# Kernel optimization log

Hardware: AMD Instinct MI355X
Metric: run time of the kernel (lower is better)

The kernel has to match this reference:

```python
import jax, jax.numpy as jnp
import numpy as np

B, T, EPROJS, DUNITS, ATT_DIM = 32, 2048, 512, 512, 512
ACONV_CHANS, ACONV_FILT = 32, 100
SCALING = 2.0


def _lin(k, fan_in, fan_out):
    k1, k2 = jax.random.split(k)
    lim = 1.0 / np.sqrt(fan_in)
    w = jax.random.uniform(k1, (fan_in, fan_out), minval=-lim, maxval=lim, dtype=jnp.float32)
    b = jax.random.uniform(k2, (fan_out,), minval=-lim, maxval=lim, dtype=jnp.float32)
    return w, b


def setup_inputs() -> dict:
    key = jax.random.key(0)
    ks = jax.random.split(key, 16)
    W_w, W_b = _lin(ks[0], DUNITS, ATT_DIM)
    V_w, V_b = _lin(ks[1], EPROJS, ATT_DIM)
    U_w, U_b = _lin(ks[2], DUNITS, ATT_DIM)
    g_w, g_b = _lin(ks[3], ATT_DIM, 1)
    K = 2 * ACONV_FILT + 1
    lim = 1.0 / np.sqrt(K)
    conv_w = jax.random.uniform(ks[4], (ACONV_CHANS, 1, K), minval=-lim, maxval=lim, dtype=jnp.float32)
    lim = 1.0 / np.sqrt(ATT_DIM)
    W_ih = jax.random.uniform(ks[5], (4 * ATT_DIM, ACONV_CHANS), minval=-lim, maxval=lim, dtype=jnp.float32)
    W_hh = jax.random.uniform(ks[6], (4 * ATT_DIM, ATT_DIM), minval=-lim, maxval=lim, dtype=jnp.float32)
    b_ih = jax.random.uniform(ks[7], (4 * ATT_DIM,), minval=-lim, maxval=lim, dtype=jnp.float32)
    b_hh = jax.random.uniform(ks[8], (4 * ATT_DIM,), minval=-lim, maxval=lim, dtype=jnp.float32)
    enc_hs_pad = jax.random.normal(ks[9], (B, T, EPROJS), dtype=jnp.float32)
    enc_hs_len = jax.random.randint(ks[10], (B,), T // 2, T + 1, dtype=jnp.int32)
    dec_z = jax.random.normal(ks[11], (B, DUNITS), dtype=jnp.float32)
    att_prev = jax.random.uniform(ks[12], (B, T), dtype=jnp.float32)
    att_h = jax.random.normal(ks[13], (B, ATT_DIM), dtype=jnp.float32)
    att_c = jax.random.normal(ks[14], (B, ATT_DIM), dtype=jnp.float32)
    return dict(enc_hs_pad=enc_hs_pad, enc_hs_len=enc_hs_len, dec_z=dec_z,
                att_prev=att_prev, att_h=att_h, att_c=att_c,
                W_w=W_w, W_b=W_b, V_w=V_w, V_b=V_b, U_w=U_w, U_b=U_b,
                g_w=g_w, g_b=g_b, conv_w=conv_w,
                W_ih=W_ih, W_hh=W_hh, b_ih=b_ih, b_hh=b_hh)


def reference(enc_hs_pad, enc_hs_len, dec_z, att_prev, att_h, att_c,
              W_w, W_b, V_w, V_b, U_w, U_b, g_w, g_b, conv_w,
              W_ih, W_hh, b_ih, b_hh):
    # pre-computed encoder projection: (B, T, att_dim)
    pre = jnp.einsum('bte,ea->bta', enc_hs_pad, V_w) + V_b
    # location conv over previous attention weights: (B, C, T)
    conv = jax.lax.conv_general_dilated(att_prev[:, None, :], conv_w,
                                        window_strides=(1,),
                                        padding=[(ACONV_FILT, ACONV_FILT)],
                                        dimension_numbers=('NCH', 'OIH', 'NCH'))
    feat = jnp.max(jax.nn.relu(conv), axis=-1)  # (B, C): max-pool over time
    # LSTMCell (torch gate order: i, f, g, o)
    gates = feat @ W_ih.T + b_ih + att_h @ W_hh.T + b_hh
    i, f, g, o = jnp.split(gates, 4, axis=-1)
    c_new = jax.nn.sigmoid(f) * att_c + jax.nn.sigmoid(i) * jnp.tanh(g)
    h_new = jax.nn.sigmoid(o) * jnp.tanh(c_new)
    # additive score
    dec_proj = dec_z @ U_w + U_b            # (B, att_dim)
    wh = h_new @ W_w + W_b                  # (B, att_dim)
    e = jnp.tanh(wh[:, None, :] + pre + dec_proj[:, None, :])  # (B, T, att_dim)
    score = jnp.einsum('bta,a->bt', e, g_w[:, 0]) + g_b[0]     # (B, T)
    mask = jnp.arange(T)[None, :] >= enc_hs_len[:, None]
    score = jnp.where(mask, jnp.asarray(-1e30, score.dtype), score)
    w = jax.nn.softmax(SCALING * score, axis=1)
    c_v = jnp.einsum('bte,bt->be', enc_hs_pad, w)  # (B, eprojs)
    return c_v, w, h_new, c_new
```

## Files before the change

kernel.cpp:

```cpp
#include <hip/hip_runtime.h>
#include <math.h>

#define BB 32
#define TT_SEQ 2048
#define EPROJS 512
#define ATT 512
#define NCH 32
#define FILT 100
#define KCONV 201
#define G4 2048

typedef unsigned short ushort_t;
typedef unsigned int uint_t;
typedef __attribute__((ext_vector_type(8))) short bf16x8_t;
typedef __attribute__((ext_vector_type(4))) float f32x4_t;

__device__ inline ushort_t f2bf(float f) {
    uint_t u = __float_as_uint(f);
    uint_t r = (u + 0x7fffu + ((u >> 16) & 1u)) >> 16;
    return (ushort_t)r;
}

__device__ inline float tanh_fast(float x) {
    float e = __expf(2.0f * x);
    return 1.0f - 2.0f / (e + 1.0f);
}

__global__ __launch_bounds__(256) void k_conv(const float* __restrict__ att_prev,
                                              const float* __restrict__ conv_w,
                                              float* __restrict__ feat) {
    int b = blockIdx.x >> 5;
    int c = blockIdx.x & 31;
    __shared__ float row[TT_SEQ + 2 * FILT];
    __shared__ float wsh[KCONV];
    __shared__ float red[4];
    for (int i = threadIdx.x; i < TT_SEQ + 2 * FILT; i += 256) {
        int t = i - FILT;
        row[i] = (t >= 0 && t < TT_SEQ) ? att_prev[b * TT_SEQ + t] : 0.0f;
    }
    for (int i = threadIdx.x; i < KCONV; i += 256) wsh[i] = conv_w[c * KCONV + i];
    __syncthreads();
    float m = 0.0f;
    for (int t = threadIdx.x; t < TT_SEQ; t += 256) {
        float s = 0.0f;
        #pragma unroll 4
        for (int k = 0; k < KCONV; ++k) s = fmaf(wsh[k], row[t + k], s);
        m = fmaxf(m, s);
    }
    #pragma unroll
    for (int off = 32; off; off >>= 1) m = fmaxf(m, __shfl_xor(m, off, 64));
    if ((threadIdx.x & 63) == 0) red[threadIdx.x >> 6] = m;
    __syncthreads();
    if (threadIdx.x == 0) {
        m = fmaxf(fmaxf(red[0], red[1]), fmaxf(red[2], red[3]));
        feat[b * NCH + c] = m;
    }
}

#define HP 518
__global__ __launch_bounds__(256) void k_gates(const float* __restrict__ feat,
                                               const float* __restrict__ att_h,
                                               const float* __restrict__ W_ih,
                                               const float* __restrict__ W_hh,
                                               const float* __restrict__ b_ih,
                                               const float* __restrict__ b_hh,
                                               float* __restrict__ gates) {
    __shared__ float hsh[32 * HP];
    __shared__ float fsh[32 * 33];
    int tid = threadIdx.x;
    for (int i = tid; i < 32 * 512; i += 256) {
        int r = i >> 9, c = i & 511;
        hsh[r * HP + c] = att_h[i];
    }
    for (int i = tid; i < 1024; i += 256) fsh[(i >> 5) * 33 + (i & 31)] = feat[i];
    __syncthreads();
    int jl = tid >> 5, b = tid & 31;
    int j = blockIdx.x * 8 + jl;
    float acc = b_ih[j] + b_hh[j];
    const float4* wi = (const float4*)(W_ih + (size_t)j * NCH);
    #pragma unroll
    for (int k4 = 0; k4 < 8; ++k4) {
        float4 w = wi[k4];
        const float* f = fsh + b * 33 + k4 * 4;
        acc = fmaf(w.x, f[0], acc);
        acc = fmaf(w.y, f[1], acc);
        acc = fmaf(w.z, f[2], acc);
        acc = fmaf(w.w, f[3], acc);
    }
    const float4* wh = (const float4*)(W_hh + (size_t)j * ATT);
    float a0 = 0.f, a1 = 0.f, a2 = 0.f, a3 = 0.f;
    #pragma unroll 8
    for (int k4 = 0; k4 < 128; ++k4) {
        float4 w = wh[k4];
        float2 h0 = *(const float2*)(hsh + b * HP + k4 * 4);
        float2 h1 = *(const float2*)(hsh + b * HP + k4 * 4 + 2);
        a0 = fmaf(w.x, h0.x, a0);
        a1 = fmaf(w.y, h0.y, a1);
        a2 = fmaf(w.z, h1.x, a2);
        a3 = fmaf(w.w, h1.y, a3);
    }
    gates[(size_t)b * G4 + j] = acc + ((a0 + a1) + (a2 + a3));
}

__global__ __launch_bounds__(256) void k_lstm_elem(const float* __restrict__ gates,
                                                   const float* __restrict__ att_c,
                                                   float* __restrict__ h_out,
                                                   float* __restrict__ c_out) {
    int i = blockIdx.x * 256 + threadIdx.x;
    int b = i >> 9, a = i & 511;
    const float* g = gates + (size_t)b * G4;
    float ig = g[a], fg = g[ATT + a], gg = g[2 * ATT + a], og = g[3 * ATT + a];
    float si = 1.0f / (1.0f + expf(-ig));
    float sf = 1.0f / (1.0f + expf(-fg));
    float so = 1.0f / (1.0f + expf(-og));
    float cn = sf * att_c[i] + si * tanhf(gg);
    float hn = so * tanhf(cn);
    c_out[i] = cn;
    h_out[i] = hn;
}

__global__ __launch_bounds__(256) void k_addvec_par(const float* __restrict__ dec_z,
                                                    const float* __restrict__ h_new,
                                                    const float* __restrict__ U_w,
                                                    const float* __restrict__ W_w,
                                                    float* __restrict__ add_vec) {
    int a0 = blockIdx.x * 32;
    int k0 = blockIdx.y * 64;
    __shared__ float zsh[32 * 65];
    __shared__ float hsh[32 * 65];
    __shared__ float us[64 * 33];
    __shared__ float ws2[64 * 33];
    int tid = threadIdx.x;
    for (int i = tid; i < 2048; i += 256) {
        int b = i >> 6, d = i & 63;
        zsh[b * 65 + d] = dec_z[(size_t)b * ATT + k0 + d];
        hsh[b * 65 + d] = h_new[(size_t)b * ATT + k0 + d];
        int dr = i >> 5, c = i & 31;
        us[dr * 33 + c] = U_w[(size_t)(k0 + dr) * ATT + a0 + c];
        ws2[dr * 33 + c] = W_w[(size_t)(k0 + dr) * ATT + a0 + c];
    }
    __syncthreads();
    int al = tid >> 5, b = tid & 31;
    float acc[4] = {0.f, 0.f, 0.f, 0.f};
    for (int d = 0; d < 64; ++d) {
        float zv = zsh[b * 65 + d];
        float hv = hsh[b * 65 + d];
        #pragma unroll
        for (int m = 0; m < 4; ++m) {
            int a = al + 8 * m;
            acc[m] = fmaf(zv, us[d * 33 + a], acc[m]);
            acc[m] = fmaf(hv, ws2[d * 33 + a], acc[m]);
        }
    }
    #pragma unroll
    for (int m = 0; m < 4; ++m)
        atomicAdd(&add_vec[(size_t)b * ATT + a0 + al + 8 * m], acc[m]);
}

__global__ __launch_bounds__(256) void k_cvt(const float* __restrict__ src,
                                             ushort_t* __restrict__ dst,
                                             float* __restrict__ score) {
    size_t i = (size_t)blockIdx.x * 256 + threadIdx.x;
    float4 v = ((const float4*)src)[i];
    ushort4 o;
    o.x = f2bf(v.x); o.y = f2bf(v.y); o.z = f2bf(v.z); o.w = f2bf(v.w);
    ((ushort4*)dst)[i] = o;
    if (i < BB * TT_SEQ) score[i] = 0.0f;
}

__global__ __launch_bounds__(256) void k_cvtw(const float* __restrict__ vw,
                                              ushort_t* __restrict__ vwt,
                                              const float* __restrict__ U_b,
                                              const float* __restrict__ W_b,
                                              const float* __restrict__ V_b,
                                              float* __restrict__ add_vec) {
    __shared__ float tile[64][65];
    int eb = blockIdx.x * 64, ab = blockIdx.y * 64;
    for (int it = 0; it < 16; ++it) {
        int idx = threadIdx.x + it * 256;
        int r = idx >> 6, c = idx & 63;
        tile[r][c] = vw[(size_t)(eb + r) * ATT + ab + c];
    }
    __syncthreads();
    for (int it = 0; it < 16; ++it) {
        int idx = threadIdx.x + it * 256;
        int r = idx >> 6, c = idx & 63;
        vwt[(size_t)(ab + r) * EPROJS + eb + c] = f2bf(tile[c][r]);
    }
    int blk = blockIdx.y * 8 + blockIdx.x;
    int i = blk * 256 + threadIdx.x;
    int a = i & 511;
    add_vec[i] = U_b[a] + W_b[a] + V_b[a];
}

__global__ __launch_bounds__(256) void k_gemm_score(
        const ushort_t* __restrict__ Abf,
        const ushort_t* __restrict__ Btbf,
        const float* __restrict__ add_vec,
        const float* __restrict__ g_w,
        const int* __restrict__ lens,
        float* __restrict__ score) {
    int mtile = blockIdx.x;
    int b = mtile >> 4;
    int t0 = (mtile & 15) * 128;
    if (t0 >= lens[b]) return;
    int n0 = blockIdx.y * 128;

    __shared__ __align__(16) ushort_t sA[128 * 64];
    __shared__ __align__(16) ushort_t sB[128 * 64];
    __shared__ float sred[128];

    int tid = threadIdx.x;
    int lane = tid & 63;
    int wave = tid >> 6;
    int wm = wave >> 1, wn = wave & 1;
    int q = lane >> 4, l15 = lane & 15;

    if (tid < 128) sred[tid] = 0.0f;

    const ushort_t* Agbase = Abf + (size_t)mtile * 128 * EPROJS;
    const ushort_t* Bgbase = Btbf + (size_t)n0 * EPROJS;

    f32x4_t acc[4][4];
    #pragma unroll
    for (int i = 0; i < 4; ++i)
        #pragma unroll
        for (int j = 0; j < 4; ++j) acc[i][j] = (f32x4_t){0.f, 0.f, 0.f, 0.f};

    for (int kc = 0; kc < 8; ++kc) {
        __syncthreads();
        #pragma unroll
        for (int it = 0; it < 4; ++it) {
            int g = tid + it * 256;
            int m = g >> 3;
            int kq = g & 7;
            int kqs = kq ^ (m & 7);
            __builtin_amdgcn_global_load_lds(
                (const __attribute__((address_space(1))) void*)(Agbase + (size_t)m * EPROJS + kc * 64 + kqs * 8),
                (__attribute__((address_space(3))) void*)(sA + g * 8), 16, 0, 0);
            __builtin_amdgcn_global_load_lds(
                (const __attribute__((address_space(1))) void*)(Bgbase + (size_t)m * EPROJS + kc * 64 + kqs * 8),
                (__attribute__((address_space(3))) void*)(sB + g * 8), 16, 0, 0);
        }
        __syncthreads();
        #pragma unroll
        for (int s = 0; s < 2; ++s) {
            bf16x8_t af[4], bfr[4];
            int kq = s * 4 + q;
            #pragma unroll
            for (int i = 0; i < 4; ++i) {
                int m = wm * 64 + i * 16 + l15;
                af[i] = *(const bf16x8_t*)(sA + (m * 8 + (kq ^ (m & 7))) * 8);
            }
            #pragma unroll
            for (int j = 0; j < 4; ++j) {
                int n = wn * 64 + j * 16 + l15;
                bfr[j] = *(const bf16x8_t*)(sB + (n * 8 + (kq ^ (n & 7))) * 8);
            }
            #pragma unroll
            for (int i = 0; i < 4; ++i)
                #pragma unroll
                for (int j = 0; j < 4; ++j)
                    acc[i][j] = __builtin_amdgcn_mfma_f32_16x16x32_bf16(af[i], bfr[j], acc[i][j], 0, 0, 0);
        }
    }

    float g4[4], av4[4];
    #pragma unroll
    for (int j = 0; j < 4; ++j) {
        int a = n0 + wn * 64 + j * 16 + l15;
        g4[j] = g_w[a];
        av4[j] = add_vec[b * ATT + a];
    }
    float s_ir[4][4];
    #pragma unroll
    for (int i = 0; i < 4; ++i) {
        #pragma unroll
        for (int r = 0; r < 4; ++r) {
            float s = 0.0f;
            #pragma unroll
            for (int j = 0; j < 4; ++j) {
                float x = acc[i][j][r] + av4[j];
                s = fmaf(g4[j], tanh_fast(x), s);
            }
            s_ir[i][r] = s;
        }
    }
    #pragma unroll
    for (int off = 8; off; off >>= 1) {
        #pragma unroll
        for (int i = 0; i < 4; ++i)
            #pragma unroll
            for (int r = 0; r < 4; ++r)
                s_ir[i][r] += __shfl_xor(s_ir[i][r], off, 16);
    }
    if (l15 == 0) {
        #pragma unroll
        for (int i = 0; i < 4; ++i)
            #pragma unroll
            for (int r = 0; r < 4; ++r)
                atomicAdd(&sred[wm * 64 + i * 16 + q * 4 + r], s_ir[i][r]);
    }
    __syncthreads();
    if (tid < 128) atomicAdd(&score[b * TT_SEQ + t0 + tid], sred[tid]);
}

__global__ __launch_bounds__(256) void k_softmax(const float* __restrict__ score,
                                                 const int* __restrict__ lens,
                                                 float* __restrict__ w_out,
                                                 float* __restrict__ c_v) {
    int b = blockIdx.x;
    int len = lens[b];
    __shared__ float red[4];
    float vals[8];
    float m = -INFINITY;
    #pragma unroll
    for (int i = 0; i < 8; ++i) {
        int t = threadIdx.x + i * 256;
        float s = (t < len) ? 2.0f * score[b * TT_SEQ + t] : -INFINITY;
        vals[i] = s;
        m = fmaxf(m, s);
    }
    #pragma unroll
    for (int off = 32; off; off >>= 1) m = fmaxf(m, __shfl_xor(m, off, 64));
    if ((threadIdx.x & 63) == 0) red[threadIdx.x >> 6] = m;
    __syncthreads();
    m = fmaxf(fmaxf(red[0], red[1]), fmaxf(red[2], red[3]));
    __syncthreads();
    float sum = 0.0f;
    #pragma unroll
    for (int i = 0; i < 8; ++i) {
        float e = expf(vals[i] - m);
        vals[i] = e;
        sum += e;
    }
    #pragma unroll
    for (int off = 32; off; off >>= 1) sum += __shfl_xor(sum, off, 64);
    if ((threadIdx.x & 63) == 0) red[threadIdx.x >> 6] = sum;
    __syncthreads();
    sum = red[0] + red[1] + red[2] + red[3];
    float inv = 1.0f / sum;
    #pragma unroll
    for (int i = 0; i < 8; ++i) w_out[b * TT_SEQ + threadIdx.x + i * 256] = vals[i] * inv;
    for (int i = threadIdx.x; i < EPROJS; i += 256) c_v[b * EPROJS + i] = 0.0f;
}

__global__ __launch_bounds__(256) void k_ctx_bf(const ushort_t* __restrict__ encb,
                                                const float* __restrict__ w,
                                                const int* __restrict__ lens,
                                                float* __restrict__ c_v) {
    int b = blockIdx.y;
    int t0 = blockIdx.x * 128;
    if (t0 >= lens[b]) return;
    __shared__ float wsh[128];
    if (threadIdx.x < 128) wsh[threadIdx.x] = w[b * TT_SEQ + t0 + threadIdx.x];
    __syncthreads();
    const uint_t* base = (const uint_t*)(encb + ((size_t)b * TT_SEQ + t0) * EPROJS);
    float a0 = 0.f, a1 = 0.f;
    for (int t = 0; t < 128; ++t) {
        uint_t u = base[t * 256 + threadIdx.x];
        float lo = __uint_as_float(u << 16);
        float hi = __uint_as_float(u & 0xffff0000u);
        a0 = fmaf(wsh[t], lo, a0);
        a1 = fmaf(wsh[t], hi, a1);
    }
    atomicAdd(&c_v[b * EPROJS + 2 * threadIdx.x], a0);
    atomicAdd(&c_v[b * EPROJS + 2 * threadIdx.x + 1], a1);
}

__global__ __launch_bounds__(256) void k_lstm(const float* __restrict__ feat,
                                              const float* __restrict__ att_h,
                                              const float* __restrict__ att_c,
                                              const float* __restrict__ W_ih,
                                              const float* __restrict__ W_hh,
                                              const float* __restrict__ b_ih,
                                              const float* __restrict__ b_hh,
                                              float* __restrict__ h_out,
                                              float* __restrict__ c_out) {
    int b = blockIdx.x;
    __shared__ float fsh[NCH];
    __shared__ float hsh[ATT];
    __shared__ float gsh[G4];
    if (threadIdx.x < NCH) fsh[threadIdx.x] = feat[b * NCH + threadIdx.x];
    for (int i = threadIdx.x; i < ATT; i += 256) hsh[i] = att_h[b * ATT + i];
    __syncthreads();
    for (int j = threadIdx.x; j < G4; j += 256) {
        float acc = b_ih[j] + b_hh[j];
        const float* wi = W_ih + (size_t)j * NCH;
        #pragma unroll
        for (int c = 0; c < NCH; ++c) acc = fmaf(fsh[c], wi[c], acc);
        const float* wh = W_hh + (size_t)j * ATT;
        for (int a = 0; a < ATT; a += 4) {
            float4 w4 = *(const float4*)(wh + a);
            acc = fmaf(hsh[a + 0], w4.x, acc);
            acc = fmaf(hsh[a + 1], w4.y, acc);
            acc = fmaf(hsh[a + 2], w4.z, acc);
            acc = fmaf(hsh[a + 3], w4.w, acc);
        }
        gsh[j] = acc;
    }
    __syncthreads();
    for (int a = threadIdx.x; a < ATT; a += 256) {
        float ig = gsh[a], fg = gsh[ATT + a], gg = gsh[2 * ATT + a], og = gsh[3 * ATT + a];
        float si = 1.0f / (1.0f + expf(-ig));
        float sf = 1.0f / (1.0f + expf(-fg));
        float so = 1.0f / (1.0f + expf(-og));
        float cn = sf * att_c[b * ATT + a] + si * tanhf(gg);
        float hn = so * tanhf(cn);
        c_out[b * ATT + a] = cn;
        h_out[b * ATT + a] = hn;
    }
}

__global__ __launch_bounds__(256) void k_addvec(const float* __restrict__ dec_z,
                                                const float* __restrict__ h_new,
                                                const float* __restrict__ U_w,
                                                const float* __restrict__ U_b,
                                                const float* __restrict__ W_w,
                                                const float* __restrict__ W_b,
                                                const float* __restrict__ V_b,
                                                float* __restrict__ add_vec) {
    int b = blockIdx.x;
    __shared__ float zsh[ATT];
    __shared__ float hsh[ATT];
    for (int i = threadIdx.x; i < ATT; i += 256) {
        zsh[i] = dec_z[b * ATT + i];
        hsh[i] = h_new[b * ATT + i];
    }
    __syncthreads();
    for (int a = threadIdx.x; a < ATT; a += 256) {
        float acc = U_b[a] + W_b[a] + V_b[a];
        for (int d = 0; d < ATT; ++d) {
            acc = fmaf(zsh[d], U_w[(size_t)d * ATT + a], acc);
            acc = fmaf(hsh[d], W_w[(size_t)d * ATT + a], acc);
        }
        add_vec[b * ATT + a] = acc;
    }
}

#define TTILE 16
#define SR 516
__global__ __launch_bounds__(256) void k_score(const float* __restrict__ enc,
                                               const float* __restrict__ V_w,
                                               const float* __restrict__ add_vec,
                                               const float* __restrict__ g_w,
                                               const float* __restrict__ g_b,
                                               const int* __restrict__ lens,
                                               float* __restrict__ score) {
    int b = blockIdx.y;
    int t0 = blockIdx.x * TTILE;
    int len = lens[b];
    if (t0 >= len) return;
    __shared__ float enc_t[TTILE * SR];
    __shared__ float ash[ATT];
    __shared__ float gwsh[ATT];
    const float* src = enc + ((size_t)b * TT_SEQ + t0) * EPROJS;
    for (int i = threadIdx.x; i < TTILE * 128; i += 256) {
        int r = i >> 7, c4 = (i & 127) << 2;
        *(float4*)(enc_t + r * SR + c4) = *(const float4*)(src + (size_t)r * EPROJS + c4);
    }
    for (int i = threadIdx.x; i < ATT; i += 256) {
        ash[i] = add_vec[b * ATT + i];
        gwsh[i] = g_w[i];
    }
    __syncthreads();
    int t = threadIdx.x >> 4;
    int al = threadIdx.x & 15;
    const float* er = enc_t + t * SR;
    float sc = 0.0f;
    #pragma unroll
    for (int c = 0; c < 2; ++c) {
        float4 acc0 = {0, 0, 0, 0}, acc1 = {0, 0, 0, 0}, acc2 = {0, 0, 0, 0}, acc3 = {0, 0, 0, 0};
        int abase = c * 256 + al * 4;
        const float* vp = V_w + abase;
        for (int e = 0; e < EPROJS; ++e) {
            float s = er[e];
            const float* rowp = vp + (size_t)e * ATT;
            float4 w0 = *(const float4*)(rowp);
            float4 w1 = *(const float4*)(rowp + 64);
            float4 w2 = *(const float4*)(rowp + 128);
            float4 w3 = *(const float4*)(rowp + 192);
            acc0.x = fmaf(s, w0.x, acc0.x); acc0.y = fmaf(s, w0.y, acc0.y);
            acc0.z = fmaf(s, w0.z, acc0.z); acc0.w = fmaf(s, w0.w, acc0.w);
            acc1.x = fmaf(s, w1.x, acc1.x); acc1.y = fmaf(s, w1.y, acc1.y);
            acc1.z = fmaf(s, w1.z, acc1.z); acc1.w = fmaf(s, w1.w, acc1.w);
            acc2.x = fmaf(s, w2.x, acc2.x); acc2.y = fmaf(s, w2.y, acc2.y);
            acc2.z = fmaf(s, w2.z, acc2.z); acc2.w = fmaf(s, w2.w, acc2.w);
            acc3.x = fmaf(s, w3.x, acc3.x); acc3.y = fmaf(s, w3.y, acc3.y);
            acc3.z = fmaf(s, w3.z, acc3.z); acc3.w = fmaf(s, w3.w, acc3.w);
        }
        float av[16] = {acc0.x, acc0.y, acc0.z, acc0.w,
                        acc1.x, acc1.y, acc1.z, acc1.w,
                        acc2.x, acc2.y, acc2.z, acc2.w,
                        acc3.x, acc3.y, acc3.z, acc3.w};
        #pragma unroll
        for (int k = 0; k < 16; ++k) {
            int a = abase + (k >> 2) * 64 + (k & 3);
            sc = fmaf(gwsh[a], tanhf(av[k] + ash[a]), sc);
        }
    }
    #pragma unroll
    for (int off = 8; off; off >>= 1) sc += __shfl_xor(sc, off, 16);
    if (al == 0) score[b * TT_SEQ + t0 + t] = sc + g_b[0];
}

__global__ __launch_bounds__(256) void k_ctx(const float* __restrict__ enc,
                                             const float* __restrict__ w,
                                             const int* __restrict__ lens,
                                             float* __restrict__ c_v) {
    int b = blockIdx.y;
    int t0 = blockIdx.x * 128;
    if (t0 >= lens[b]) return;
    __shared__ float wsh[128];
    if (threadIdx.x < 128) wsh[threadIdx.x] = w[b * TT_SEQ + t0 + threadIdx.x];
    __syncthreads();
    float a0 = 0.0f, a1 = 0.0f;
    const float* base = enc + ((size_t)b * TT_SEQ + t0) * EPROJS;
    for (int t = 0; t < 128; ++t) {
        float wt = wsh[t];
        a0 = fmaf(wt, base[(size_t)t * EPROJS + threadIdx.x], a0);
        a1 = fmaf(wt, base[(size_t)t * EPROJS + threadIdx.x + 256], a1);
    }
    atomicAdd(&c_v[b * EPROJS + threadIdx.x], a0);
    atomicAdd(&c_v[b * EPROJS + threadIdx.x + 256], a1);
}

extern "C" void kernel_launch(void* const* d_in, const int* in_sizes, int n_in,
                              void* d_out, int out_size, void* d_ws, size_t ws_size,
                              hipStream_t stream) {
    const float* enc      = (const float*)d_in[0];
    const int*   lens     = (const int*)d_in[1];
    const float* dec_z    = (const float*)d_in[2];
    const float* att_prev = (const float*)d_in[3];
    const float* att_h    = (const float*)d_in[4];
    const float* att_c    = (const float*)d_in[5];
    const float* W_w      = (const float*)d_in[6];
    const float* W_b      = (const float*)d_in[7];
    const float* V_w      = (const float*)d_in[8];
    const float* V_b      = (const float*)d_in[9];
    const float* U_w      = (const float*)d_in[10];
    const float* U_b      = (const float*)d_in[11];
    const float* g_w      = (const float*)d_in[12];
    const float* g_b      = (const float*)d_in[13];
    const float* conv_w   = (const float*)d_in[14];
    const float* W_ih     = (const float*)d_in[15];
    const float* W_hh     = (const float*)d_in[16];
    const float* b_ih     = (const float*)d_in[17];
    const float* b_hh     = (const float*)d_in[18];

    float* out   = (float*)d_out;
    float* c_v   = out;
    float* w_out = out + BB * EPROJS;
    float* h_out = w_out + BB * TT_SEQ;
    float* c_out = h_out + BB * ATT;

    const size_t ENC_N = (size_t)BB * TT_SEQ * EPROJS;
    const size_t need = ENC_N * 2 + (size_t)ATT * EPROJS * 2 +
                        (size_t)(1024 + BB * ATT + BB * TT_SEQ + BB * G4) * sizeof(float);

    if (ws_size >= need) {
        ushort_t* encb = (ushort_t*)d_ws;
        ushort_t* vwt  = encb + ENC_N;
        float* feat    = (float*)(vwt + (size_t)ATT * EPROJS);
        float* add_vec = feat + 1024;
        float* score   = add_vec + BB * ATT;
        float* gates   = score + BB * TT_SEQ;

        k_cvt<<<dim3(ENC_N / 4 / 256), dim3(256), 0, stream>>>(enc, encb, score);
        k_cvtw<<<dim3(8, 8), dim3(256), 0, stream>>>(V_w, vwt, U_b, W_b, V_b, add_vec);
        k_conv<<<dim3(BB * NCH), dim3(256), 0, stream>>>(att_prev, conv_w, feat);
        k_gates<<<dim3(G4 / 8), dim3(256), 0, stream>>>(feat, att_h, W_ih, W_hh,
                                                        b_ih, b_hh, gates);
        k_lstm_elem<<<dim3(64), dim3(256), 0, stream>>>(gates, att_c, h_out, c_out);
        k_addvec_par<<<dim3(16, 8), dim3(256), 0, stream>>>(dec_z, h_out, U_w, W_w, add_vec);
        k_gemm_score<<<dim3(512, 4), dim3(256), 0, stream>>>(encb, vwt, add_vec, g_w,
                                                             lens, score);
        k_softmax<<<dim3(BB), dim3(256), 0, stream>>>(score, lens, w_out, c_v);
        k_ctx_bf<<<dim3(16, BB), dim3(256), 0, stream>>>(encb, w_out, lens, c_v);
    } else {
        float* ws      = (float*)d_ws;
        float* feat    = ws;
        float* add_vec = ws + 1024;
        float* score   = ws + 1024 + BB * ATT;

        k_conv<<<dim3(BB * NCH), dim3(256), 0, stream>>>(att_prev, conv_w, feat);
        k_lstm<<<dim3(BB), dim3(256), 0, stream>>>(feat, att_h, att_c, W_ih, W_hh,
                                                   b_ih, b_hh, h_out, c_out);
        k_addvec<<<dim3(BB), dim3(256), 0, stream>>>(dec_z, h_out, U_w, U_b, W_w, W_b,
                                                     V_b, add_vec);
        k_score<<<dim3(TT_SEQ / TTILE, BB), dim3(256), 0, stream>>>(enc, V_w, add_vec,
                                                                    g_w, g_b, lens, score);
        k_softmax<<<dim3(BB), dim3(256), 0, stream>>>(score, lens, w_out, c_v);
        k_ctx<<<dim3(16, BB), dim3(256), 0, stream>>>(enc, w_out, lens, c_v);
    }
}
```

Before: 399.7 us.

## Widen score GEMM to full N per block, register-block conv, finer ctx split

The score GEMM now has each 512-thread block cover all 512 attention columns. The A tile is loaded once per block instead of four times, the tanh/g_w reduction finishes in-block, and the score is written directly, so neither the score-zeroing pass in the conversion kernel nor the global atomics are needed. The conv kernel has each thread compute eight outputs with a sliding window of float4 LDS loads, reading weights from global/scalar memory. The context kernel splits time into 64-step chunks to launch twice as many blocks. The wider GEMM tile needs 80KB of LDS and more accumulator registers, which limits occupancy.

Measured after the change: 348.5 us. 1.15x faster.

```diff
diff --git a/kernel.cpp b/kernel.cpp
--- a/kernel.cpp
+++ b/kernel.cpp
@@ -31,22 +31,41 @@
                                               float* __restrict__ feat) {
     int b = blockIdx.x >> 5;
     int c = blockIdx.x & 31;
-    __shared__ float row[TT_SEQ + 2 * FILT];
-    __shared__ float wsh[KCONV];
+    __shared__ __align__(16) float row[TT_SEQ + 2 * FILT + 8];
     __shared__ float red[4];
-    for (int i = threadIdx.x; i < TT_SEQ + 2 * FILT; i += 256) {
+    for (int i = threadIdx.x; i < TT_SEQ + 2 * FILT + 8; i += 256) {
         int t = i - FILT;
         row[i] = (t >= 0 && t < TT_SEQ) ? att_prev[b * TT_SEQ + t] : 0.0f;
     }
-    for (int i = threadIdx.x; i < KCONV; i += 256) wsh[i] = conv_w[c * KCONV + i];
-    __syncthreads();
+    __syncthreads();
+    const float* cw = conv_w + c * KCONV;
+    int t0 = threadIdx.x * 8;
+    float acc[8] = {0.f, 0.f, 0.f, 0.f, 0.f, 0.f, 0.f, 0.f};
+    float4 r0 = *(const float4*)(row + t0);
+    float4 r1 = *(const float4*)(row + t0 + 4);
+    float r[8] = {r0.x, r0.y, r0.z, r0.w, r1.x, r1.y, r1.z, r1.w};
+    for (int k = 0; k < 200; k += 8) {
+        float4 n0 = *(const float4*)(row + t0 + k + 8);
+        float4 n1 = *(const float4*)(row + t0 + k + 12);
+        float nn[8] = {n0.x, n0.y, n0.z, n0.w, n1.x, n1.y, n1.z, n1.w};
+        #pragma unroll
+        for (int kk = 0; kk < 8; ++kk) {
+            float w = cw[k + kk];
+            #pragma unroll
+            for (int i = 0; i < 8; ++i) {
+                float rv = (kk + i < 8) ? r[kk + i] : nn[kk + i - 8];
+                acc[i] = fmaf(w, rv, acc[i]);
+            }
+        }
+        #pragma unroll
+        for (int i = 0; i < 8; ++i) r[i] = nn[i];
+    }
+    float wlast = cw[200];
+    #pragma unroll
+    for (int i = 0; i < 8; ++i) acc[i] = fmaf(wlast, r[i], acc[i]);
     float m = 0.0f;
-    for (int t = threadIdx.x; t < TT_SEQ; t += 256) {
-        float s = 0.0f;
-        #pragma unroll 4
-        for (int k = 0; k < KCONV; ++k) s = fmaf(wsh[k], row[t + k], s);
-        m = fmaxf(m, s);
-    }
+    #pragma unroll
+    for (int i = 0; i < 8; ++i) m = fmaxf(m, acc[i]);
     #pragma unroll
     for (int off = 32; off; off >>= 1) m = fmaxf(m, __shfl_xor(m, off, 64));
     if ((threadIdx.x & 63) == 0) red[threadIdx.x >> 6] = m;
@@ -158,14 +177,12 @@
 }
 
 __global__ __launch_bounds__(256) void k_cvt(const float* __restrict__ src,
-                                             ushort_t* __restrict__ dst,
-                                             float* __restrict__ score) {
+                                             ushort_t* __restrict__ dst) {
     size_t i = (size_t)blockIdx.x * 256 + threadIdx.x;
     float4 v = ((const float4*)src)[i];
     ushort4 o;
     o.x = f2bf(v.x); o.y = f2bf(v.y); o.z = f2bf(v.z); o.w = f2bf(v.w);
     ((ushort4*)dst)[i] = o;
-    if (i < BB * TT_SEQ) score[i] = 0.0f;
 }
 
 __global__ __launch_bounds__(256) void k_cvtw(const float* __restrict__ vw,
@@ -193,7 +210,7 @@
     add_vec[i] = U_b[a] + W_b[a] + V_b[a];
 }
 
-__global__ __launch_bounds__(256) void k_gemm_score(
+__global__ __launch_bounds__(512, 2) void k_gemm_score2(
         const ushort_t* __restrict__ Abf,
         const ushort_t* __restrict__ Btbf,
         const float* __restrict__ add_vec,
@@ -204,48 +221,50 @@
     int b = mtile >> 4;
     int t0 = (mtile & 15) * 128;
     if (t0 >= lens[b]) return;
-    int n0 = blockIdx.y * 128;
 
     __shared__ __align__(16) ushort_t sA[128 * 64];
-    __shared__ __align__(16) ushort_t sB[128 * 64];
-    __shared__ float sred[128];
+    __shared__ __align__(16) ushort_t sB[512 * 64];
 
     int tid = threadIdx.x;
     int lane = tid & 63;
     int wave = tid >> 6;
-    int wm = wave >> 1, wn = wave & 1;
+    int wm = wave >> 2, wn = wave & 3;
     int q = lane >> 4, l15 = lane & 15;
 
-    if (tid < 128) sred[tid] = 0.0f;
-
-    const ushort_t* Agbase = Abf + (size_t)mtile * 128 * EPROJS;
-    const ushort_t* Bgbase = Btbf + (size_t)n0 * EPROJS;
-
-    f32x4_t acc[4][4];
+    const ushort_t* Ag = Abf + (size_t)mtile * 128 * EPROJS;
+
+    f32x4_t acc[4][8];
     #pragma unroll
     for (int i = 0; i < 4; ++i)
         #pragma unroll
-        for (int j = 0; j < 4; ++j) acc[i][j] = (f32x4_t){0.f, 0.f, 0.f, 0.f};
+        for (int j = 0; j < 8; ++j) acc[i][j] = (f32x4_t){0.f, 0.f, 0.f, 0.f};
 
     for (int kc = 0; kc < 8; ++kc) {
         __syncthreads();
         #pragma unroll
-        for (int it = 0; it < 4; ++it) {
-            int g = tid + it * 256;
+        for (int it = 0; it < 2; ++it) {
+            int g = tid + it * 512;
             int m = g >> 3;
             int kq = g & 7;
             int kqs = kq ^ (m & 7);
             __builtin_amdgcn_global_load_lds(
-                (const __attribute__((address_space(1))) void*)(Agbase + (size_t)m * EPROJS + kc * 64 + kqs * 8),
+                (const __attribute__((address_space(1))) void*)(Ag + (size_t)m * EPROJS + kc * 64 + kqs * 8),
                 (__attribute__((address_space(3))) void*)(sA + g * 8), 16, 0, 0);
+        }
+        #pragma unroll
+        for (int it = 0; it < 8; ++it) {
+            int g = tid + it * 512;
+            int n = g >> 3;
+            int kq = g & 7;
+            int kqs = kq ^ (n & 7);
             __builtin_amdgcn_global_load_lds(
-                (const __attribute__((address_space(1))) void*)(Bgbase + (size_t)m * EPROJS + kc * 64 + kqs * 8),
+                (const __attribute__((address_space(1))) void*)(Btbf + (size_t)n * EPROJS + kc * 64 + kqs * 8),
                 (__attribute__((address_space(3))) void*)(sB + g * 8), 16, 0, 0);
         }
         __syncthreads();
         #pragma unroll
         for (int s = 0; s < 2; ++s) {
-            bf16x8_t af[4], bfr[4];
+            bf16x8_t af[4], bfr[8];
             int kq = s * 4 + q;
             #pragma unroll
             for (int i = 0; i < 4; ++i) {
@@ -253,24 +272,24 @@
                 af[i] = *(const bf16x8_t*)(sA + (m * 8 + (kq ^ (m & 7))) * 8);
             }
             #pragma unroll
-            for (int j = 0; j < 4; ++j) {
-                int n = wn * 64 + j * 16 + l15;
+            for (int j = 0; j < 8; ++j) {
+                int n = wn * 128 + j * 16 + l15;
                 bfr[j] = *(const bf16x8_t*)(sB + (n * 8 + (kq ^ (n & 7))) * 8);
             }
             #pragma unroll
             for (int i = 0; i < 4; ++i)
                 #pragma unroll
-                for (int j = 0; j < 4; ++j)
+                for (int j = 0; j < 8; ++j)
                     acc[i][j] = __builtin_amdgcn_mfma_f32_16x16x32_bf16(af[i], bfr[j], acc[i][j], 0, 0, 0);
         }
     }
 
-    float g4[4], av4[4];
-    #pragma unroll
-    for (int j = 0; j < 4; ++j) {
-        int a = n0 + wn * 64 + j * 16 + l15;
-        g4[j] = g_w[a];
-        av4[j] = add_vec[b * ATT + a];
+    float g8[8], av8[8];
+    #pragma unroll
+    for (int j = 0; j < 8; ++j) {
+        int a = wn * 128 + j * 16 + l15;
+        g8[j] = g_w[a];
+        av8[j] = add_vec[b * ATT + a];
     }
     float s_ir[4][4];
     #pragma unroll
@@ -279,9 +298,9 @@
         for (int r = 0; r < 4; ++r) {
             float s = 0.0f;
             #pragma unroll
-            for (int j = 0; j < 4; ++j) {
-                float x = acc[i][j][r] + av4[j];
-                s = fmaf(g4[j], tanh_fast(x), s);
+            for (int j = 0; j < 8; ++j) {
+                float x = acc[i][j][r] + av8[j];
+                s = fmaf(g8[j], tanh_fast(x), s);
             }
             s_ir[i][r] = s;
         }
@@ -294,6 +313,10 @@
             for (int r = 0; r < 4; ++r)
                 s_ir[i][r] += __shfl_xor(s_ir[i][r], off, 16);
     }
+    __syncthreads();
+    float* sred = (float*)sA;
+    if (tid < 128) sred[tid] = 0.0f;
+    __syncthreads();
     if (l15 == 0) {
         #pragma unroll
         for (int i = 0; i < 4; ++i)
@@ -302,7 +325,7 @@
                 atomicAdd(&sred[wm * 64 + i * 16 + q * 4 + r], s_ir[i][r]);
     }
     __syncthreads();
-    if (tid < 128) atomicAdd(&score[b * TT_SEQ + t0 + tid], sred[tid]);
+    if (tid < 128) score[b * TT_SEQ + t0 + tid] = sred[tid];
 }
 
 __global__ __launch_bounds__(256) void k_softmax(const float* __restrict__ score,
@@ -350,14 +373,14 @@
                                                 const int* __restrict__ lens,
                                                 float* __restrict__ c_v) {
     int b = blockIdx.y;
-    int t0 = blockIdx.x * 128;
+    int t0 = blockIdx.x * 64;
     if (t0 >= lens[b]) return;
-    __shared__ float wsh[128];
-    if (threadIdx.x < 128) wsh[threadIdx.x] = w[b * TT_SEQ + t0 + threadIdx.x];
+    __shared__ float wsh[64];
+    if (threadIdx.x < 64) wsh[threadIdx.x] = w[b * TT_SEQ + t0 + threadIdx.x];
     __syncthreads();
     const uint_t* base = (const uint_t*)(encb + ((size_t)b * TT_SEQ + t0) * EPROJS);
     float a0 = 0.f, a1 = 0.f;
-    for (int t = 0; t < 128; ++t) {
+    for (int t = 0; t < 64; ++t) {
         uint_t u = base[t * 256 + threadIdx.x];
         float lo = __uint_as_float(u << 16);
         float hi = __uint_as_float(u & 0xffff0000u);
@@ -566,17 +589,17 @@
         float* score   = add_vec + BB * ATT;
         float* gates   = score + BB * TT_SEQ;
 
-        k_cvt<<<dim3(ENC_N / 4 / 256), dim3(256), 0, stream>>>(enc, encb, score);
+        k_cvt<<<dim3(ENC_N / 4 / 256), dim3(256), 0, stream>>>(enc, encb);
         k_cvtw<<<dim3(8, 8), dim3(256), 0, stream>>>(V_w, vwt, U_b, W_b, V_b, add_vec);
         k_conv<<<dim3(BB * NCH), dim3(256), 0, stream>>>(att_prev, conv_w, feat);
         k_gates<<<dim3(G4 / 8), dim3(256), 0, stream>>>(feat, att_h, W_ih, W_hh,
                                                         b_ih, b_hh, gates);
         k_lstm_elem<<<dim3(64), dim3(256), 0, stream>>>(gates, att_c, h_out, c_out);
         k_addvec_par<<<dim3(16, 8), dim3(256), 0, stream>>>(dec_z, h_out, U_w, W_w, add_vec);
-        k_gemm_score<<<dim3(512, 4), dim3(256), 0, stream>>>(encb, vwt, add_vec, g_w,
-                                                             lens, score);
+        k_gemm_score2<<<dim3(512), dim3(512), 0, stream>>>(encb, vwt, add_vec, g_w,
+                                                           lens, score);
         k_softmax<<<dim3(BB), dim3(256), 0, stream>>>(score, lens, w_out, c_v);
-        k_ctx_bf<<<dim3(16, BB), dim3(256), 0, stream>>>(encb, w_out, lens, c_v);
+        k_ctx_bf<<<dim3(32, BB), dim3(256), 0, stream>>>(encb, w_out, lens, c_v);
     } else {
         float* ws      = (float*)d_ws;
         float* feat    = ws;
```
